# Optimization experiments

Hardware: AMD Instinct MI355X
Metric: run time of the kernel (lower is better)

## Reference

```python
import jax, jax.numpy as jnp
import numpy as np
from jax import lax

N, OC, IC, K = 32, 256, 256, 3
H = W = 56
STRIDE = 1
PADDING = 1
SPARSITY = 0.9  # fraction of zero weights


def setup_inputs() -> dict:
    key = jax.random.key(0)
    k_in, k_w, k_b, k_m = jax.random.split(key, 4)
    input = jax.random.normal(k_in, (N, IC, H, W), dtype=jnp.float32)
    weight = jax.random.normal(k_w, (OC, IC, K, K), dtype=jnp.float32) * 0.05
    bias = jax.random.normal(k_b, (OC,), dtype=jnp.float32) * 0.05
    mask = jax.random.bernoulli(k_m, p=1.0 - SPARSITY, shape=(OC, IC, K, K))
    return {"input": input, "weight": weight, "bias": bias, "mask": mask}


def reference(input, weight, bias, mask):
    # SparseConv2d stores only nonzero weights (W_val at W_idx); mathematically this
    # is a dense conv2d with the masked weight tensor.
    w = jnp.where(mask, weight, jnp.zeros((), dtype=weight.dtype))
    out = lax.conv_general_dilated(
        input, w,
        window_strides=(STRIDE, STRIDE),
        padding=[(PADDING, PADDING), (PADDING, PADDING)],
        dimension_numbers=("NCHW", "OIHW", "NCHW"),
    )
    return out + bias[None, :, None, None]
```

## Files before the change

### kernel.cpp

```cpp
#include <hip/hip_runtime.h>

constexpr int NB=32, ICC=256, OCC=256, HH=56, WW=56;
constexpr int HW=HH*WW, CHW=ICC*HW;
constexpr int YT=14;
constexpr int BUFB = 6*58*64;
constexpr int ROWB = 58*64;
constexpr int LROW=58;
constexpr int PAD=36;
constexpr int LDS_ELEMS=6*LROW*PAD;

using short8  = __attribute__((ext_vector_type(8))) short;
using short4v = __attribute__((ext_vector_type(4))) short;
using f32x4   = __attribute__((ext_vector_type(4))) float;

__device__ inline unsigned bf16rne(float x){
  unsigned u = __float_as_uint(x);
  return (u + 0x7fffu + ((u>>16)&1u)) >> 16;
}

__global__ __launch_bounds__(256) void pack_weights(
    const float* __restrict__ w, const int* __restrict__ mask,
    unsigned short* __restrict__ wb){
  const int oc = blockIdx.x, ic = threadIdx.x;
  const int base = (oc*ICC + ic)*9;
  #pragma unroll
  for (int j=0;j<9;++j){
    float v = (mask[base+j] != 0) ? w[base+j] : 0.f;
    wb[(j*OCC + oc)*ICC + ic] = (unsigned short)bf16rne(v);
  }
}

__global__ __launch_bounds__(256) void pack_input(
    const float* __restrict__ in, unsigned short* __restrict__ inb){
  __shared__ unsigned t2[56*130];
  const int bid = blockIdx.x;
  const int n = bid/56, y = bid - n*56;
  const float* src = in + (size_t)n*CHW + y*WW;
  const int tid = threadIdx.x;
  #pragma unroll
  for (int i=0;i<7;++i){
    int idx = tid + i*256;
    int icp = idx / 14, xg = idx - icp*14;
    const float* gp = src + (2*icp)*HW + xg*4;
    float4 g0 = *(const float4*)gp;
    float4 g1 = *(const float4*)(gp + HW);
    int xb = xg*4;
    t2[(xb+0)*130 + icp] = bf16rne(g0.x) | (bf16rne(g1.x)<<16);
    t2[(xb+1)*130 + icp] = bf16rne(g0.y) | (bf16rne(g1.y)<<16);
    t2[(xb+2)*130 + icp] = bf16rne(g0.z) | (bf16rne(g1.z)<<16);
    t2[(xb+3)*130 + icp] = bf16rne(g0.w) | (bf16rne(g1.w)<<16);
  }
  __syncthreads();
  unsigned* dst = (unsigned*)(inb + (size_t)(n*56+y)*56*256);
  #pragma unroll
  for (int i=0;i<28;++i){
    int idx = tid + i*256;
    int x = idx >> 7, icp = idx & 127;
    dst[idx] = t2[x*130 + icp];
  }
}

__global__ __launch_bounds__(256,1) void conv_mfma(
    const unsigned short* __restrict__ inb, const unsigned short* __restrict__ wb,
    const float* __restrict__ bias, float* __restrict__ out){
  __shared__ __align__(16) unsigned short xt[2*6*58*32];

  const int lid  = blockIdx.x;
  const int xcd  = lid & 7, slot = lid >> 3;
  const int ngrp = slot / 14, yt = slot - ngrp*14;
  const int n    = xcd + 8*ngrp;
  const int y0   = yt*4;

  const int tid  = threadIdx.x;
  const int lane = tid & 63, wv = tid >> 6;
  const int q    = lane >> 4, l16 = lane & 15;

  const int ocw = (wv & 1)*128;
  const int pxw = (wv >> 1)*112;

  int base2[7][3];
  #pragma unroll
  for (int p=0;p<7;++p){
    int px = pxw + p*16 + l16;
    int yl = px / 56, x = px - yl*56;
    #pragma unroll
    for (int kw=0;kw<3;++kw){
      int c = x + kw;
      base2[p][kw] = yl*ROWB + c*64 + ((q ^ ((c>>1)&3))<<4);
    }
  }

  f32x4 acc[8][7];
  #pragma unroll
  for (int s=0;s<8;++s)
    #pragma unroll
    for (int p=0;p<7;++p) acc[s][p] = (f32x4){0.f,0.f,0.f,0.f};

  const int rskipA = (yt==0)      ? 0 : -1;
  const int rskipB = (yt==YT-1)   ? 5 : -1;

  const unsigned short* nb = inb + (size_t)n*(56*56*256);

  auto stage = [&](int buf, int ch){
    const int ic0 = ch*32;
    #pragma unroll
    for (int i=0;i<6;++i){
      int t   = wv*6 + i;
      int row = t >> 2, k = t & 3;
      if (row != rskipA && row != rskipB){
        int ir = k*64 + lane;
        int cc = ir >> 2, sub = ir & 3;
        int icg = sub ^ (((cc+1)>>1)&3);
        int y  = y0 - 1 + row;
        const unsigned short* gp = nb + (y*56 + cc)*256 + ic0 + icg*8;
        char* lp = (char*)xt + buf*BUFB + (row*58 + 1)*64 + ir*16;
        if (ir < 224)
          __builtin_amdgcn_global_load_lds(
              (const __attribute__((address_space(1))) void*)gp,
              (__attribute__((address_space(3))) void*)lp, 16, 0, 0);
      }
    }
  };

  auto compute = [&](int buf, int ch){
    const int ic0 = ch*32;
    const char* xb = (const char*)xt + buf*BUFB;
    const unsigned short* wpb = wb + (ocw + l16)*ICC + ic0 + q*8;
    short8 a0 = *(const short8*)(wpb           );
    short8 a1 = *(const short8*)(wpb +  16*ICC );
    short8 a2 = *(const short8*)(wpb +  32*ICC );
    short8 a3 = *(const short8*)(wpb +  48*ICC );
    short8 a4 = *(const short8*)(wpb +  64*ICC );
    short8 a5 = *(const short8*)(wpb +  80*ICC );
    short8 a6 = *(const short8*)(wpb +  96*ICC );
    short8 a7 = *(const short8*)(wpb + 112*ICC );
    #pragma unroll
    for (int j=0;j<9;++j){
      short8 n0,n1,n2,n3,n4,n5,n6,n7;
      if (j < 8){
        const unsigned short* wn = wpb + (j+1)*OCC*ICC;
        n0 = *(const short8*)(wn           );
        n1 = *(const short8*)(wn +  16*ICC );
        n2 = *(const short8*)(wn +  32*ICC );
        n3 = *(const short8*)(wn +  48*ICC );
        n4 = *(const short8*)(wn +  64*ICC );
        n5 = *(const short8*)(wn +  80*ICC );
        n6 = *(const short8*)(wn +  96*ICC );
        n7 = *(const short8*)(wn + 112*ICC );
      }
      const int kh = j/3, kw = j - kh*3;
      const int doff = kh*ROWB;
      #pragma unroll
      for (int p=0;p<7;++p){
        short8 b = *(const short8*)(xb + base2[p][kw] + doff);
        acc[0][p] = __builtin_amdgcn_mfma_f32_16x16x32_bf16(a0, b, acc[0][p], 0,0,0);
        acc[1][p] = __builtin_amdgcn_mfma_f32_16x16x32_bf16(a1, b, acc[1][p], 0,0,0);
        acc[2][p] = __builtin_amdgcn_mfma_f32_16x16x32_bf16(a2, b, acc[2][p], 0,0,0);
        acc[3][p] = __builtin_amdgcn_mfma_f32_16x16x32_bf16(a3, b, acc[3][p], 0,0,0);
        acc[4][p] = __builtin_amdgcn_mfma_f32_16x16x32_bf16(a4, b, acc[4][p], 0,0,0);
        acc[5][p] = __builtin_amdgcn_mfma_f32_16x16x32_bf16(a5, b, acc[5][p], 0,0,0);
        acc[6][p] = __builtin_amdgcn_mfma_f32_16x16x32_bf16(a6, b, acc[6][p], 0,0,0);
        acc[7][p] = __builtin_amdgcn_mfma_f32_16x16x32_bf16(a7, b, acc[7][p], 0,0,0);
      }
      if (j < 8){ a0=n0;a1=n1;a2=n2;a3=n3;a4=n4;a5=n5;a6=n6;a7=n7; }
    }
  };

  #pragma unroll 4
  for (int i = tid; i < 2*BUFB/16; i += 256) ((f32x4*)xt)[i] = (f32x4){0.f,0.f,0.f,0.f};
  __syncthreads();

  stage(0, 0);
  __syncthreads();

  for (int ch=0; ch<8; ++ch){
    if (ch < 7) stage((ch+1)&1, ch+1);
    compute(ch&1, ch);
    __syncthreads();
  }

  #pragma unroll
  for (int s=0;s<8;++s){
    const int oc4 = ocw + s*16 + q*4;
    float4 bv = *(const float4*)(bias + oc4);
    #pragma unroll
    for (int i=0;i<4;++i){
      const float bb = (i==0)?bv.x:(i==1)?bv.y:(i==2)?bv.z:bv.w;
      float* op = out + (n*OCC + oc4 + i)*HW + y0*WW + pxw + l16;
      #pragma unroll
      for (int p=0;p<7;++p){
        op[p*16] = acc[s][p][i] + bb;
      }
    }
  }
}

__global__ __launch_bounds__(256,2) void conv_mfma_f32(
    const float* __restrict__ in, const unsigned short* __restrict__ wb,
    const float* __restrict__ bias, float* __restrict__ out){
  __shared__ unsigned short xt[LDS_ELEMS];

  const int lid  = blockIdx.x;
  const int xcd  = lid & 7, slot = lid >> 3;
  const int ngrp = slot / 28, rem = slot - ngrp*28;
  const int mt   = rem / 14,  yt  = rem - mt*14;
  const int n    = xcd + 8*ngrp;
  const int y0   = yt*4, ocb = mt*128;

  const int tid  = threadIdx.x;
  const int lane = tid & 63, wv = tid >> 6;
  const int q    = lane >> 4, l16 = lane & 15;

  for (int i = tid; i < LDS_ELEMS/2; i += 256) ((unsigned*)xt)[i] = 0u;

  const int ocw = ocb + (wv & 1)*64;
  const int pxw = (wv >> 1)*112;

  int pbase[7];
  #pragma unroll
  for (int p=0;p<7;++p){
    int px = pxw + p*16 + l16;
    int ylv = px / 56, x = px - ylv*56;
    pbase[p] = (ylv*LROW + x)*(PAD*2) + q*16;
  }

  f32x4 acc[4][7];
  #pragma unroll
  for (int s=0;s<4;++s)
    #pragma unroll
    for (int p=0;p<7;++p) acc[s][p] = (f32x4){0.f,0.f,0.f,0.f};

  const int rskipA = (yt==0)      ? 0 : -1;
  const int rskipB = (yt==YT-1)   ? 5 : -1;

  __syncthreads();

  for (int ch=0; ch<8; ++ch){
    const int ic0 = ch*32;
    #pragma unroll
    for (int i=0;i<6;++i){
      int idx = tid + i*256;
      if (idx < 1344){
        int r  = idx / 224;
        int r2 = idx - r*224;
        int xg = r2 >> 4, icp = r2 & 15;
        if (r != rskipA && r != rskipB){
          int y = y0 - 1 + r;
          const float* gp = in + n*CHW + (ic0 + icp*2)*HW + y*WW + xg*4;
          float4 g0 = *(const float4*)gp;
          float4 g1 = *(const float4*)(gp + HW);
          unsigned w0 = bf16rne(g0.x) | (bf16rne(g1.x)<<16);
          unsigned w1 = bf16rne(g0.y) | (bf16rne(g1.y)<<16);
          unsigned w2 = bf16rne(g0.z) | (bf16rne(g1.z)<<16);
          unsigned w3 = bf16rne(g0.w) | (bf16rne(g1.w)<<16);
          unsigned* dp = (unsigned*)xt + (r*LROW + 1 + xg*4)*(PAD/2) + icp;
          dp[0]         = w0;
          dp[PAD/2]     = w1;
          dp[PAD]       = w2;
          dp[3*(PAD/2)] = w3;
        }
      }
    }
    __syncthreads();

    #pragma unroll
    for (int kh=0;kh<3;++kh){
      #pragma unroll
      for (int kw=0;kw<3;++kw){
        const int j = kh*3 + kw;
        const unsigned short* wp = wb + (j*OCC + ocw + l16)*ICC + ic0 + q*8;
        short8 a0 = *(const short8*)(wp          );
        short8 a1 = *(const short8*)(wp + 16*ICC );
        short8 a2 = *(const short8*)(wp + 32*ICC );
        short8 a3 = *(const short8*)(wp + 48*ICC );
        const int doff = (kh*LROW + kw)*(PAD*2);
        #pragma unroll
        for (int p=0;p<7;++p){
          const char* bp = (const char*)xt + pbase[p] + doff;
          short4v blo = *(const short4v*)(bp    );
          short4v bhi = *(const short4v*)(bp + 8);
          short8 b = __builtin_shufflevector(blo, bhi, 0,1,2,3,4,5,6,7);
          acc[0][p] = __builtin_amdgcn_mfma_f32_16x16x32_bf16(a0, b, acc[0][p], 0,0,0);
          acc[1][p] = __builtin_amdgcn_mfma_f32_16x16x32_bf16(a1, b, acc[1][p], 0,0,0);
          acc[2][p] = __builtin_amdgcn_mfma_f32_16x16x32_bf16(a2, b, acc[2][p], 0,0,0);
          acc[3][p] = __builtin_amdgcn_mfma_f32_16x16x32_bf16(a3, b, acc[3][p], 0,0,0);
        }
      }
    }
    __syncthreads();
  }

  #pragma unroll
  for (int s=0;s<4;++s){
    const int oc4 = ocw + s*16 + q*4;
    float4 bv = *(const float4*)(bias + oc4);
    #pragma unroll
    for (int i=0;i<4;++i){
      const float bb = (i==0)?bv.x:(i==1)?bv.y:(i==2)?bv.z:bv.w;
      float* op = out + (n*OCC + oc4 + i)*HW + y0*WW + pxw + l16;
      #pragma unroll
      for (int p=0;p<7;++p){
        op[p*16] = acc[s][p][i] + bb;
      }
    }
  }
}

extern "C" void kernel_launch(void* const* d_in, const int* in_sizes, int n_in,
                              void* d_out, int out_size, void* d_ws, size_t ws_size,
                              hipStream_t stream) {
  const float* in   = (const float*)d_in[0];
  const float* w    = (const float*)d_in[1];
  const float* bias = (const float*)d_in[2];
  const int*   mask = (const int*)d_in[3];
  float*       out  = (float*)d_out;
  unsigned short* wb = (unsigned short*)d_ws;

  const size_t WB_BYTES  = (size_t)9*OCC*ICC*2;
  const size_t INB_BYTES = (size_t)NB*HH*WW*ICC*2;

  pack_weights<<<OCC, 256, 0, stream>>>(w, mask, wb);
  if (ws_size >= WB_BYTES + INB_BYTES){
    unsigned short* inb = (unsigned short*)((char*)d_ws + WB_BYTES);
    pack_input<<<NB*HH, 256, 0, stream>>>(in, inb);
    conv_mfma<<<8*56, 256, 0, stream>>>(inb, wb, bias, out);
  } else {
    conv_mfma_f32<<<8*4*2*YT, 256, 0, stream>>>(in, wb, bias, out);
  }
}
```

Baseline: 385.9 us.

## Restructure conv MFMA kernel to 512 threads with 128-channel single-buffer stages

The main conv kernel moves from 256-thread blocks with 8 double-buffered 32-channel stages to 512-thread blocks (8 waves, 64 output channels each) that stage 128 input channels at a time into one LDS buffer, in two phases. The LDS layout changes to 256-byte cells with an XOR swizzle over 8 slots, and only the halo edges are zeroed instead of the whole buffer. This cuts per-wave accumulators in half to allow two blocks per CU and reduces the number of barriers. In exchange, the global-to-LDS loads no longer overlap compute, and weights are reloaded per 32-channel sub-chunk with no prefetch.

Measured after the change: 417.6 us. +8.2%, slower.

```diff
diff --git a/kernel.cpp b/kernel.cpp
--- a/kernel.cpp
+++ b/kernel.cpp
@@ -2,9 +2,11 @@
 
 constexpr int NB=32, ICC=256, OCC=256, HH=56, WW=56;
 constexpr int HW=HH*WW, CHW=ICC*HW;
+constexpr int STRIPS=14;
+constexpr int CELLB=256;
+constexpr int ROWB2=58*CELLB;
+constexpr int XTB=6*ROWB2;
 constexpr int YT=14;
-constexpr int BUFB = 6*58*64;
-constexpr int ROWB = 58*64;
 constexpr int LROW=58;
 constexpr int PAD=36;
 constexpr int LDS_ELEMS=6*LROW*PAD;
@@ -60,25 +62,25 @@
   }
 }
 
-__global__ __launch_bounds__(256,1) void conv_mfma(
+__global__ __launch_bounds__(512,2) void conv_mfma(
     const unsigned short* __restrict__ inb, const unsigned short* __restrict__ wb,
     const float* __restrict__ bias, float* __restrict__ out){
-  __shared__ __align__(16) unsigned short xt[2*6*58*32];
+  __shared__ __align__(16) unsigned short xt[XTB/2];
 
   const int lid  = blockIdx.x;
   const int xcd  = lid & 7, slot = lid >> 3;
-  const int ngrp = slot / 14, yt = slot - ngrp*14;
+  const int ngrp = slot / STRIPS, strip = slot - ngrp*STRIPS;
   const int n    = xcd + 8*ngrp;
-  const int y0   = yt*4;
+  const int y0   = strip*4;
 
   const int tid  = threadIdx.x;
   const int lane = tid & 63, wv = tid >> 6;
   const int q    = lane >> 4, l16 = lane & 15;
 
-  const int ocw = (wv & 1)*128;
-  const int pxw = (wv >> 1)*112;
-
-  int base2[7][3];
+  const int ocw = (wv & 3)*64;
+  const int pxw = (wv >> 2)*112;
+
+  int cb[7][3], xm[7][3];
   #pragma unroll
   for (int p=0;p<7;++p){
     int px = pxw + p*16 + l16;
@@ -86,101 +88,86 @@
     #pragma unroll
     for (int kw=0;kw<3;++kw){
       int c = x + kw;
-      base2[p][kw] = yl*ROWB + c*64 + ((q ^ ((c>>1)&3))<<4);
-    }
-  }
-
-  f32x4 acc[8][7];
-  #pragma unroll
-  for (int s=0;s<8;++s)
+      cb[p][kw] = yl*ROWB2 + c*CELLB;
+      xm[p][kw] = c & 7;
+    }
+  }
+
+  f32x4 acc[4][7];
+  #pragma unroll
+  for (int s=0;s<4;++s)
     #pragma unroll
     for (int p=0;p<7;++p) acc[s][p] = (f32x4){0.f,0.f,0.f,0.f};
 
-  const int rskipA = (yt==0)      ? 0 : -1;
-  const int rskipB = (yt==YT-1)   ? 5 : -1;
+  const int rskipA = (strip==0)         ? 0 : -1;
+  const int rskipB = (strip==STRIPS-1)  ? 5 : -1;
 
   const unsigned short* nb = inb + (size_t)n*(56*56*256);
 
-  auto stage = [&](int buf, int ch){
-    const int ic0 = ch*32;
-    #pragma unroll
-    for (int i=0;i<6;++i){
-      int t   = wv*6 + i;
-      int row = t >> 2, k = t & 3;
-      if (row != rskipA && row != rskipB){
-        int ir = k*64 + lane;
-        int cc = ir >> 2, sub = ir & 3;
-        int icg = sub ^ (((cc+1)>>1)&3);
-        int y  = y0 - 1 + row;
-        const unsigned short* gp = nb + (y*56 + cc)*256 + ic0 + icg*8;
-        char* lp = (char*)xt + buf*BUFB + (row*58 + 1)*64 + ir*16;
-        if (ir < 224)
+  const f32x4 z4 = (f32x4){0.f,0.f,0.f,0.f};
+  if (tid < 192){
+    int row = tid/32, t2 = tid & 31, cs = t2>>4, i16 = t2 & 15;
+    *(f32x4*)((char*)xt + row*ROWB2 + cs*57*CELLB + i16*16) = z4;
+  }
+  if (strip==0)        for (int i=tid;i<ROWB2/16;i+=512) *(f32x4*)((char*)xt + i*16) = z4;
+  if (strip==STRIPS-1) for (int i=tid;i<ROWB2/16;i+=512) *(f32x4*)((char*)xt + 5*ROWB2 + i*16) = z4;
+
+  auto stage = [&](int ic0){
+    #pragma unroll
+    for (int i=0;i<11;++i){
+      int idx = tid + i*512;
+      if (idx < 5376){
+        int r = idx / 896;
+        if (r != rskipA && r != rskipB){
+          int rm = idx - r*896;
+          int c_in = rm >> 4, s = rm & 15;
+          int y = y0 - 1 + r;
+          int g = s ^ ((1 + c_in) & 7);
+          const unsigned short* gp = nb + (y*56 + c_in)*256 + ic0 + g*8;
+          char* lp = (char*)xt + idx*16 + r*512 + 256;
           __builtin_amdgcn_global_load_lds(
               (const __attribute__((address_space(1))) void*)gp,
               (__attribute__((address_space(3))) void*)lp, 16, 0, 0);
+        }
       }
     }
   };
 
-  auto compute = [&](int buf, int ch){
-    const int ic0 = ch*32;
-    const char* xb = (const char*)xt + buf*BUFB;
-    const unsigned short* wpb = wb + (ocw + l16)*ICC + ic0 + q*8;
-    short8 a0 = *(const short8*)(wpb           );
-    short8 a1 = *(const short8*)(wpb +  16*ICC );
-    short8 a2 = *(const short8*)(wpb +  32*ICC );
-    short8 a3 = *(const short8*)(wpb +  48*ICC );
-    short8 a4 = *(const short8*)(wpb +  64*ICC );
-    short8 a5 = *(const short8*)(wpb +  80*ICC );
-    short8 a6 = *(const short8*)(wpb +  96*ICC );
-    short8 a7 = *(const short8*)(wpb + 112*ICC );
+  auto compute = [&](int ic0){
     #pragma unroll
     for (int j=0;j<9;++j){
-      short8 n0,n1,n2,n3,n4,n5,n6,n7;
-      if (j < 8){
-        const unsigned short* wn = wpb + (j+1)*OCC*ICC;
-        n0 = *(const short8*)(wn           );
-        n1 = *(const short8*)(wn +  16*ICC );
-        n2 = *(const short8*)(wn +  32*ICC );
-        n3 = *(const short8*)(wn +  48*ICC );
-        n4 = *(const short8*)(wn +  64*ICC );
-        n5 = *(const short8*)(wn +  80*ICC );
-        n6 = *(const short8*)(wn +  96*ICC );
-        n7 = *(const short8*)(wn + 112*ICC );
-      }
       const int kh = j/3, kw = j - kh*3;
-      const int doff = kh*ROWB;
+      const unsigned short* wj = wb + (j*OCC + ocw + l16)*ICC + ic0 + q*8;
       #pragma unroll
-      for (int p=0;p<7;++p){
-        short8 b = *(const short8*)(xb + base2[p][kw] + doff);
-        acc[0][p] = __builtin_amdgcn_mfma_f32_16x16x32_bf16(a0, b, acc[0][p], 0,0,0);
-        acc[1][p] = __builtin_amdgcn_mfma_f32_16x16x32_bf16(a1, b, acc[1][p], 0,0,0);
-        acc[2][p] = __builtin_amdgcn_mfma_f32_16x16x32_bf16(a2, b, acc[2][p], 0,0,0);
-        acc[3][p] = __builtin_amdgcn_mfma_f32_16x16x32_bf16(a3, b, acc[3][p], 0,0,0);
-        acc[4][p] = __builtin_amdgcn_mfma_f32_16x16x32_bf16(a4, b, acc[4][p], 0,0,0);
-        acc[5][p] = __builtin_amdgcn_mfma_f32_16x16x32_bf16(a5, b, acc[5][p], 0,0,0);
-        acc[6][p] = __builtin_amdgcn_mfma_f32_16x16x32_bf16(a6, b, acc[6][p], 0,0,0);
-        acc[7][p] = __builtin_amdgcn_mfma_f32_16x16x32_bf16(a7, b, acc[7][p], 0,0,0);
-      }
-      if (j < 8){ a0=n0;a1=n1;a2=n2;a3=n3;a4=n4;a5=n5;a6=n6;a7=n7; }
+      for (int c8=0;c8<4;++c8){
+        const unsigned short* wc = wj + c8*32;
+        short8 a0 = *(const short8*)(wc          );
+        short8 a1 = *(const short8*)(wc + 16*ICC );
+        short8 a2 = *(const short8*)(wc + 32*ICC );
+        short8 a3 = *(const short8*)(wc + 48*ICC );
+        #pragma unroll
+        for (int p=0;p<7;++p){
+          int slt = ((c8<<2) | q) ^ xm[p][kw];
+          short8 b = *(const short8*)((char*)xt + cb[p][kw] + kh*ROWB2 + (slt<<4));
+          acc[0][p] = __builtin_amdgcn_mfma_f32_16x16x32_bf16(a0, b, acc[0][p], 0,0,0);
+          acc[1][p] = __builtin_amdgcn_mfma_f32_16x16x32_bf16(a1, b, acc[1][p], 0,0,0);
+          acc[2][p] = __builtin_amdgcn_mfma_f32_16x16x32_bf16(a2, b, acc[2][p], 0,0,0);
+          acc[3][p] = __builtin_amdgcn_mfma_f32_16x16x32_bf16(a3, b, acc[3][p], 0,0,0);
+        }
+      }
     }
   };
 
-  #pragma unroll 4
-  for (int i = tid; i < 2*BUFB/16; i += 256) ((f32x4*)xt)[i] = (f32x4){0.f,0.f,0.f,0.f};
-  __syncthreads();
-
-  stage(0, 0);
-  __syncthreads();
-
-  for (int ch=0; ch<8; ++ch){
-    if (ch < 7) stage((ch+1)&1, ch+1);
-    compute(ch&1, ch);
-    __syncthreads();
-  }
-
-  #pragma unroll
-  for (int s=0;s<8;++s){
+  stage(0);
+  __syncthreads();
+  compute(0);
+  __syncthreads();
+  stage(128);
+  __syncthreads();
+  compute(128);
+
+  #pragma unroll
+  for (int s=0;s<4;++s){
     const int oc4 = ocw + s*16 + q*4;
     float4 bv = *(const float4*)(bias + oc4);
     #pragma unroll
@@ -323,7 +310,7 @@
   if (ws_size >= WB_BYTES + INB_BYTES){
     unsigned short* inb = (unsigned short*)((char*)d_ws + WB_BYTES);
     pack_input<<<NB*HH, 256, 0, stream>>>(in, inb);
-    conv_mfma<<<8*56, 256, 0, stream>>>(inb, wb, bias, out);
+    conv_mfma<<<8*4*STRIPS, 512, 0, stream>>>(inb, wb, bias, out);
   } else {
     conv_mfma_f32<<<8*4*2*YT, 256, 0, stream>>>(in, wb, bias, out);
   }
```
